# Kernel tuning notes

Hardware: AMD Instinct MI355X
Metric: run time of the kernel (lower is better)

## Reference

```python
import jax, jax.numpy as jnp
import numpy as np

N_NODES = 100000
N_EDGES = 1600000
D = 128
K = 3
LAMBDA_MAX = 2.0  # PyG ChebConv default for normalization='sym'


def _cheb_conv(x, row, col, w, diag, lins, bias):
    # x: [N, D]; w: [E] scaled-Laplacian off-diag weights; diag: scalar diag weight
    # lins: [K, D, D]; bias: [D]
    n = x.shape[0]

    def prop(v):
        # out[col] += w * v[row]  (sparse L_hat @ v), plus diagonal term
        return jax.ops.segment_sum(w[:, None] * v[row], col, num_segments=n) + diag * v

    Tx0 = x
    out = Tx0 @ lins[0]
    Tx1 = prop(Tx0)
    out = out + Tx1 @ lins[1]
    for k in range(2, lins.shape[0]):
        Tx2 = 2.0 * prop(Tx1) - Tx0
        out = out + Tx2 @ lins[k]
        Tx0, Tx1 = Tx1, Tx2
    return out + bias


def setup_inputs() -> dict:
    key = jax.random.key(0)
    ks = jax.random.split(key, 10)
    glorot = float(np.sqrt(6.0 / (D + D)))
    X = jax.random.normal(ks[0], (N_NODES, D), dtype=jnp.float32)
    edge_index = jax.random.randint(ks[1], (2, N_EDGES), 0, N_NODES, dtype=jnp.int64)
    edge_weight = jax.random.uniform(ks[2], (N_EDGES,), dtype=jnp.float32)
    H = jax.random.normal(ks[3], (N_NODES, D), dtype=jnp.float32)
    C = jax.random.normal(ks[4], (N_NODES, D), dtype=jnp.float32)
    # gate order: i, f, c, o
    W = jax.random.uniform(ks[5], (4, D, D), dtype=jnp.float32, minval=-glorot, maxval=glorot)
    b = jnp.zeros((4, D), dtype=jnp.float32)
    conv_W = jax.random.uniform(ks[6], (4, K, D, D), dtype=jnp.float32, minval=-glorot, maxval=glorot)
    conv_b = jnp.zeros((4, D), dtype=jnp.float32)
    return {"X": X, "edge_index": edge_index, "edge_weight": edge_weight,
            "H": H, "C": C, "W": W, "b": b, "conv_W": conv_W, "conv_b": conv_b}


def reference(X, edge_index, edge_weight, H, C, W, b, conv_W, conv_b):
    n = X.shape[0]
    row, col = edge_index[0], edge_index[1]
    # sym-normalized Laplacian, scaled: L_hat = 2L/lmax - I
    deg = jax.ops.segment_sum(edge_weight, row, num_segments=n)
    dinv = jnp.where(deg > 0, deg ** -0.5, 0.0)
    w = -(dinv[row] * edge_weight * dinv[col]) * (2.0 / LAMBDA_MAX)
    diag = 2.0 / LAMBDA_MAX - 1.0  # scalar (0.0 when lmax == 2)

    def gate(g):
        return X @ W[g] + _cheb_conv(H, row, col, w, diag, conv_W[g], conv_b[g]) + b[g]

    I = jax.nn.sigmoid(gate(0))
    F = jax.nn.sigmoid(gate(1))
    T = jnp.tanh(gate(2))
    C_new = F * C + I * T
    O = jax.nn.sigmoid(gate(3))
    H_new = O * jnp.tanh(C_new)
    return H_new
```

## Files before the change

kernel.cpp:

```cpp
#include <hip/hip_runtime.h>

#define N_NODES 100000
#define N_EDGES 1600000
#define CAP 64

typedef unsigned short ushort_t;
typedef __attribute__((ext_vector_type(8))) short bf16x8;
typedef __attribute__((ext_vector_type(4))) float f32x4;
typedef __attribute__((ext_vector_type(4))) int int4e;
typedef __attribute__((ext_vector_type(4))) unsigned short ushort4e;

__device__ __forceinline__ unsigned short f2bf(float f) {
  unsigned int u = __float_as_uint(f);
  u = (u + 0x7FFFu + ((u >> 16) & 1u)) >> 16;
  return (unsigned short)u;
}

__global__ __launch_bounds__(256) void k_misc(
    const int* __restrict__ ei, const float* __restrict__ ew,
    const float* __restrict__ X, const float* __restrict__ H,
    float* __restrict__ deg, int* __restrict__ cnt, int2* __restrict__ bE,
    ushort_t* __restrict__ U,
    const float* __restrict__ W, const float* __restrict__ b,
    const float* __restrict__ cW, const float* __restrict__ cb,
    ushort_t* __restrict__ Bt, float* __restrict__ bias) {
  int bid = blockIdx.x;
  int role = bid & 7, q = bid >> 3;
  if (role < 2) {
    int e = (q * 2 + role) * 256 + threadIdx.x;
    if (e < N_EDGES) atomicAdd(&deg[ei[e]], ew[e]);
  } else if (role < 4) {
    int e = (q * 2 + (role - 2)) * 256 + threadIdx.x;
    if (e < N_EDGES) {
      int r = ei[e], c = ei[N_EDGES + e];
      float w = ew[e];
      int pos = atomicAdd(&cnt[c], 1);
      if (pos < CAP) bE[c * CAP + pos] = make_int2(r, __float_as_int(w));
    }
  } else {
    int s = q * 4 + (role - 4);
    if (s < 12500) {
      int i = s * 256 + threadIdx.x;
      int n = i >> 5, qq = i & 31;
      float4 x = *(const float4*)(X + (size_t)n * 128 + qq * 4);
      float4 h = *(const float4*)(H + (size_t)n * 128 + qq * 4);
      ushort4 a, bb;
      a.x = f2bf(x.x); a.y = f2bf(x.y); a.z = f2bf(x.z); a.w = f2bf(x.w);
      bb.x = f2bf(h.x); bb.y = f2bf(h.y); bb.z = f2bf(h.z); bb.w = f2bf(h.w);
      *(ushort4*)(U + (size_t)n * 512 + qq * 4) = a;
      *(ushort4*)(U + (size_t)n * 512 + 128 + qq * 4) = bb;
    } else if (s < 13524) {
      int idx = (s - 12500) * 256 + threadIdx.x;
      int j = idx >> 9, k = idx & 511;
      int dd = j >> 2, g = j & 3;
      float v;
      if (k < 128) v = W[(g * 128 + k) * 128 + dd];
      else {
        int kk = k - 128;
        int blk = kk >> 7;
        v = cW[((g * 3 + blk) * 128 + (kk & 127)) * 128 + dd];
      }
      Bt[idx] = f2bf(v);
      if (k == 0) bias[j] = b[g * 128 + dd] + cb[g * 128 + dd];
    }
  }
}

__global__ __launch_bounds__(256) void k_scale(
    const int* __restrict__ cnt, const float* __restrict__ deg,
    int2* __restrict__ bE) {
  int slot = blockIdx.x * 256 + threadIdx.x;
  int node = slot >> 6, i = slot & 63;
  int cn = cnt[node]; if (cn > CAP) cn = CAP;
  if (i < cn) {
    int2 p = bE[slot];
    float d = deg[p.x];
    float w = d > 0.f ? rsqrtf(d) * __int_as_float(p.y) : 0.f;
    bE[slot].y = __float_as_int(w);
  }
}

#define FMA4(A, W, V) \
  A.x = fmaf(W, V.x, A.x); A.y = fmaf(W, V.y, A.y); \
  A.z = fmaf(W, V.z, A.z); A.w = fmaf(W, V.w, A.w);

#define GATH(vv, p) { \
  ushort4 rw = *(const ushort4*)(sb + (size_t)(p) * 512); \
  vv.x = __uint_as_float((unsigned)rw.x << 16); \
  vv.y = __uint_as_float((unsigned)rw.y << 16); \
  vv.z = __uint_as_float((unsigned)rw.z << 16); \
  vv.w = __uint_as_float((unsigned)rw.w << 16); }

template <int PHASE>
__global__ __launch_bounds__(256) void k_gather(
    const int* __restrict__ cnt, const int2* __restrict__ bE,
    const float* __restrict__ deg, const float* __restrict__ H,
    ushort_t* __restrict__ U) {
  int g = threadIdx.x >> 5, lane = threadIdx.x & 31;
  int node = blockIdx.x * 8 + g;
  if (node >= N_NODES) return;
  int cn = cnt[node]; if (cn > CAP) cn = CAP;
  const int2* be = bE + node * CAP;
  const ushort_t* sb = U + (PHASE == 1 ? 128 : 256) + lane * 4;
  float dc = deg[node];
  float sc = dc > 0.f ? -rsqrtf(dc) : 0.f;

  float4 z = {0.f, 0.f, 0.f, 0.f};
  float4 a0 = z, a1 = z, a2 = z, a3 = z, a4 = z, a5 = z, a6 = z, a7 = z;
  int i = 0;
  for (; i + 8 <= cn; i += 8) {
    int4e p0 = __builtin_nontemporal_load((const int4e*)(be + i));
    int4e p1 = __builtin_nontemporal_load((const int4e*)(be + i + 2));
    int4e p2 = __builtin_nontemporal_load((const int4e*)(be + i + 4));
    int4e p3 = __builtin_nontemporal_load((const int4e*)(be + i + 6));
    float4 v0, v1, v2, v3, v4, v5, v6, v7;
    GATH(v0, p0.x); GATH(v1, p0.z); GATH(v2, p1.x); GATH(v3, p1.z);
    GATH(v4, p2.x); GATH(v5, p2.z); GATH(v6, p3.x); GATH(v7, p3.z);
    FMA4(a0, __int_as_float(p0.y), v0); FMA4(a1, __int_as_float(p0.w), v1);
    FMA4(a2, __int_as_float(p1.y), v2); FMA4(a3, __int_as_float(p1.w), v3);
    FMA4(a4, __int_as_float(p2.y), v4); FMA4(a5, __int_as_float(p2.w), v5);
    FMA4(a6, __int_as_float(p3.y), v6); FMA4(a7, __int_as_float(p3.w), v7);
  }
  for (; i + 4 <= cn; i += 4) {
    int4e p0 = __builtin_nontemporal_load((const int4e*)(be + i));
    int4e p1 = __builtin_nontemporal_load((const int4e*)(be + i + 2));
    float4 v0, v1, v2, v3;
    GATH(v0, p0.x); GATH(v1, p0.z); GATH(v2, p1.x); GATH(v3, p1.z);
    FMA4(a0, __int_as_float(p0.y), v0); FMA4(a1, __int_as_float(p0.w), v1);
    FMA4(a2, __int_as_float(p1.y), v2); FMA4(a3, __int_as_float(p1.w), v3);
  }
  for (; i < cn; ++i) {
    int2 p = be[i];
    float4 v;
    GATH(v, p.x);
    FMA4(a0, __int_as_float(p.y), v);
  }
  float4 acc;
  acc.x = sc * (((a0.x + a1.x) + (a2.x + a3.x)) + ((a4.x + a5.x) + (a6.x + a7.x)));
  acc.y = sc * (((a0.y + a1.y) + (a2.y + a3.y)) + ((a4.y + a5.y) + (a6.y + a7.y)));
  acc.z = sc * (((a0.z + a1.z) + (a2.z + a3.z)) + ((a4.z + a5.z) + (a6.z + a7.z)));
  acc.w = sc * (((a0.w + a1.w) + (a2.w + a3.w)) + ((a4.w + a5.w) + (a6.w + a7.w)));

  if (PHASE == 1) {
    ushort4e u = {f2bf(acc.x), f2bf(acc.y), f2bf(acc.z), f2bf(acc.w)};
    __builtin_nontemporal_store(u, (ushort4e*)(U + (size_t)node * 512 + 256 + lane * 4));
  } else {
    float4 h = *(const float4*)(H + (size_t)node * 128 + lane * 4);
    ushort4e u = {f2bf(2.f * acc.x - h.x), f2bf(2.f * acc.y - h.y),
                  f2bf(2.f * acc.z - h.z), f2bf(2.f * acc.w - h.w)};
    __builtin_nontemporal_store(u, (ushort4e*)(U + (size_t)node * 512 + 384 + lane * 4));
  }
}

__global__ __launch_bounds__(256) void k_gemm(
    const ushort_t* __restrict__ U, const ushort_t* __restrict__ Bt,
    const float* __restrict__ bias, const float* __restrict__ C,
    float* __restrict__ out) {
  __shared__ char ldsRaw[65536];
  char* ldsA0 = ldsRaw;
  char* ldsB0 = ldsRaw + 16384;
  char* ldsA1 = ldsRaw + 32768;
  char* ldsB1 = ldsRaw + 49152;
  float* ldsF = (float*)ldsRaw;

  const int tid = threadIdx.x;
  const int lane = tid & 63;
  const int w = tid >> 6;
  const int wr = w >> 1, wc = w & 1;
  const int b = blockIdx.x;
  const int g = (b & 7) * 391 + (b >> 3);
  const int m0 = (g >> 2) * 128;
  const int n0 = (g & 3) * 128;
  const int l15 = lane & 15;
  const int l4 = lane >> 4;

  auto stage_half = [&](int kt, char* la_base, char* lb_base, int h) {
    const int k0 = kt * 64;
#pragma unroll
    for (int is = 2 * h; is < 2 * h + 2; ++is) {
      int s = is * 256 + tid;
      int row = s >> 3;
      int cs = (s & 7) ^ (row & 7);
      const ushort_t* ga = U + (size_t)(m0 + row) * 512 + k0 + cs * 8;
      const ushort_t* gb = Bt + (size_t)(n0 + row) * 512 + k0 + cs * 8;
      char* la = la_base + (is * 256 + (tid & 192)) * 16;
      char* lb = lb_base + (is * 256 + (tid & 192)) * 16;
      __builtin_amdgcn_global_load_lds((const __attribute__((address_space(1))) void*)ga,
                                       (__attribute__((address_space(3))) void*)la, 16, 0, 0);
      __builtin_amdgcn_global_load_lds((const __attribute__((address_space(1))) void*)gb,
                                       (__attribute__((address_space(3))) void*)lb, 16, 0, 0);
    }
  };

  const int fcol = tid & 31;
  const int rbase = tid >> 5;
  float cpre[16];
#pragma unroll
  for (int half = 0; half < 2; ++half)
#pragma unroll
    for (int k = 0; k < 8; ++k) {
      int n = m0 + half * 64 + rbase + k * 8;
      int dg = (n0 >> 2) + fcol;
      cpre[half * 8 + k] = (n < N_NODES)
          ? __builtin_nontemporal_load(C + (size_t)n * 128 + dg) : 0.f;
    }

  int offA[2][4], offB[2][4];
#pragma unroll
  for (int ks = 0; ks < 2; ++ks) {
    int slot = ((ks * 4 + l4) ^ (l15 & 7)) * 16;
#pragma unroll
    for (int i = 0; i < 4; ++i) {
      offA[ks][i] = (wr * 64 + i * 16 + l15) * 128 + slot;
      offB[ks][i] = (wc * 64 + i * 16 + l15) * 128 + slot;
    }
  }

  f32x4 acc[4][4] = {};

  stage_half(0, ldsA0, ldsB0, 0);
  stage_half(0, ldsA0, ldsB0, 1);

  for (int kt = 0; kt < 8; ++kt) {
    char* curA = (kt & 1) ? ldsA1 : ldsA0;
    char* curB = (kt & 1) ? ldsB1 : ldsB0;
    char* nA = (kt & 1) ? ldsA0 : ldsA1;
    char* nB = (kt & 1) ? ldsB0 : ldsB1;
    if (kt < 7) {
      stage_half(kt + 1, nA, nB, 0);
      asm volatile("s_waitcnt vmcnt(4)" ::: "memory");
    } else {
      asm volatile("s_waitcnt vmcnt(0)" ::: "memory");
    }
    __builtin_amdgcn_s_barrier();
    __builtin_amdgcn_sched_barrier(0);

    {
      bf16x8 af[4], bfr[4];
#pragma unroll
      for (int mi = 0; mi < 4; ++mi) af[mi] = *(const bf16x8*)(curA + offA[0][mi]);
#pragma unroll
      for (int ni = 0; ni < 4; ++ni) bfr[ni] = *(const bf16x8*)(curB + offB[0][ni]);
      asm volatile("s_waitcnt lgkmcnt(0)" ::: "memory");
      __builtin_amdgcn_sched_barrier(0);
      __builtin_amdgcn_s_setprio(1);
#pragma unroll
      for (int mi = 0; mi < 4; ++mi)
#pragma unroll
        for (int ni = 0; ni < 4; ++ni)
          acc[mi][ni] = __builtin_amdgcn_mfma_f32_16x16x32_bf16(af[mi], bfr[ni], acc[mi][ni], 0, 0, 0);
      __builtin_amdgcn_s_setprio(0);
    }
    if (kt < 7) stage_half(kt + 1, nA, nB, 1);
    {
      bf16x8 af[4], bfr[4];
#pragma unroll
      for (int mi = 0; mi < 4; ++mi) af[mi] = *(const bf16x8*)(curA + offA[1][mi]);
#pragma unroll
      for (int ni = 0; ni < 4; ++ni) bfr[ni] = *(const bf16x8*)(curB + offB[1][ni]);
      asm volatile("s_waitcnt lgkmcnt(0)" ::: "memory");
      __builtin_amdgcn_sched_barrier(0);
      __builtin_amdgcn_s_setprio(1);
#pragma unroll
      for (int mi = 0; mi < 4; ++mi)
#pragma unroll
        for (int ni = 0; ni < 4; ++ni)
          acc[mi][ni] = __builtin_amdgcn_mfma_f32_16x16x32_bf16(af[mi], bfr[ni], acc[mi][ni], 0, 0, 0);
      __builtin_amdgcn_s_setprio(0);
    }
    __builtin_amdgcn_s_barrier();
  }

#pragma unroll
  for (int half = 0; half < 2; ++half) {
    if (wr == half) {
#pragma unroll
      for (int ni = 0; ni < 4; ++ni) {
        int col = wc * 64 + ni * 16 + l15;
        float bv = bias[n0 + col];
#pragma unroll
        for (int mi = 0; mi < 4; ++mi)
#pragma unroll
          for (int r = 0; r < 4; ++r)
            ldsF[(mi * 16 + l4 * 4 + r) * 132 + col] = acc[mi][ni][r] + bv;
      }
    }
    __syncthreads();
#pragma unroll
    for (int k = 0; k < 8; ++k) {
      int p = tid + k * 256;
      int rl = p >> 5, f = p & 31;
      int n = m0 + half * 64 + rl;
      if (n < N_NODES) {
        float4 pre = *(const float4*)&ldsF[rl * 132 + f * 4];
        int dg = (n0 >> 2) + f;
        float ig = __builtin_amdgcn_rcpf(1.f + __expf(-pre.x));
        float fg = __builtin_amdgcn_rcpf(1.f + __expf(-pre.y));
        float ec = __expf(-2.f * fabsf(pre.z));
        float tg = __builtin_copysignf((1.f - ec) * __builtin_amdgcn_rcpf(1.f + ec), pre.z);
        float og = __builtin_amdgcn_rcpf(1.f + __expf(-pre.w));
        float cOld = cpre[half * 8 + k];
        float cn = fg * cOld + ig * tg;
        float en = __expf(-2.f * fabsf(cn));
        float th = __builtin_copysignf((1.f - en) * __builtin_amdgcn_rcpf(1.f + en), cn);
        __builtin_nontemporal_store(og * th, out + (size_t)n * 128 + dg);
      }
    }
    __syncthreads();
  }
}

extern "C" void kernel_launch(void* const* d_in, const int* in_sizes, int n_in,
                              void* d_out, int out_size, void* d_ws, size_t ws_size,
                              hipStream_t stream) {
  const float* X  = (const float*)d_in[0];
  const int*   ei = (const int*)d_in[1];
  const float* ew = (const float*)d_in[2];
  const float* H  = (const float*)d_in[3];
  const float* C  = (const float*)d_in[4];
  const float* W  = (const float*)d_in[5];
  const float* b  = (const float*)d_in[6];
  const float* cW = (const float*)d_in[7];
  const float* cb = (const float*)d_in[8];
  float* out = (float*)d_out;
  char* ws = (char*)d_ws;

  float*    deg  = (float*)(ws);
  int*      cnt  = (int*)(ws + 0x80000);
  int2*     bE   = (int2*)(ws + 0x100000);
  ushort_t* U    = (ushort_t*)(ws + 0x3500000);
  ushort_t* Bt   = (ushort_t*)(ws + 0x9700000);
  float*    bias = (float*)(ws + 0x9780000);

  hipMemsetAsync(ws, 0, 0x100000, stream);

  k_misc<<<27128, 256, 0, stream>>>(ei, ew, X, H, deg, cnt, bE, U, W, b, cW, cb, Bt, bias);
  k_scale<<<N_NODES * CAP / 256, 256, 0, stream>>>(cnt, deg, bE);
  k_gather<1><<<(N_NODES + 7) / 8, 256, 0, stream>>>(cnt, bE, deg, H, U);
  k_gather<2><<<(N_NODES + 7) / 8, 256, 0, stream>>>(cnt, bE, deg, H, U);
  k_gemm<<<3128, 256, 0, stream>>>(U, Bt, bias, C, out);
}
```

Baseline: 449.8 us.

## Widen gather loads to 16 bytes per lane and split degree atomics into two arrays

The gather kernel now assigns 16 lanes per node, each loading 8 bf16 values (16 bytes) per neighbor row instead of 4, so each block processes twice as many nodes and issues fewer, wider loads. The degree accumulation is split across two partial arrays written by different block roles, and a new small kernel sums them, with the aim of reducing atomic contention. The change adds an extra kernel launch and larger memset, and doubles per-thread accumulator registers, which may lower occupancy.

```diff
diff --git a/kernel.cpp b/kernel.cpp
--- a/kernel.cpp
+++ b/kernel.cpp
@@ -8,7 +8,7 @@
 typedef __attribute__((ext_vector_type(8))) short bf16x8;
 typedef __attribute__((ext_vector_type(4))) float f32x4;
 typedef __attribute__((ext_vector_type(4))) int int4e;
-typedef __attribute__((ext_vector_type(4))) unsigned short ushort4e;
+typedef __attribute__((ext_vector_type(8))) unsigned short ushort8e;
 
 __device__ __forceinline__ unsigned short f2bf(float f) {
   unsigned int u = __float_as_uint(f);
@@ -19,7 +19,8 @@
 __global__ __launch_bounds__(256) void k_misc(
     const int* __restrict__ ei, const float* __restrict__ ew,
     const float* __restrict__ X, const float* __restrict__ H,
-    float* __restrict__ deg, int* __restrict__ cnt, int2* __restrict__ bE,
+    float* __restrict__ degc0, float* __restrict__ degc1,
+    int* __restrict__ cnt, int2* __restrict__ bE,
     ushort_t* __restrict__ U,
     const float* __restrict__ W, const float* __restrict__ b,
     const float* __restrict__ cW, const float* __restrict__ cb,
@@ -28,7 +29,10 @@
   int role = bid & 7, q = bid >> 3;
   if (role < 2) {
     int e = (q * 2 + role) * 256 + threadIdx.x;
-    if (e < N_EDGES) atomicAdd(&deg[ei[e]], ew[e]);
+    if (e < N_EDGES) {
+      float* dg = role ? degc1 : degc0;
+      atomicAdd(&dg[ei[e]], ew[e]);
+    }
   } else if (role < 4) {
     int e = (q * 2 + (role - 2)) * 256 + threadIdx.x;
     if (e < N_EDGES) {
@@ -66,6 +70,13 @@
   }
 }
 
+__global__ __launch_bounds__(256) void k_sumdeg(
+    const float* __restrict__ degc0, const float* __restrict__ degc1,
+    float* __restrict__ deg) {
+  int i = blockIdx.x * 256 + threadIdx.x;
+  deg[i] = degc0[i] + degc1[i];
+}
+
 __global__ __launch_bounds__(256) void k_scale(
     const int* __restrict__ cnt, const float* __restrict__ deg,
     int2* __restrict__ bE) {
@@ -80,75 +91,86 @@
   }
 }
 
-#define FMA4(A, W, V) \
-  A.x = fmaf(W, V.x, A.x); A.y = fmaf(W, V.y, A.y); \
-  A.z = fmaf(W, V.z, A.z); A.w = fmaf(W, V.w, A.w);
-
-#define GATH(vv, p) { \
-  ushort4 rw = *(const ushort4*)(sb + (size_t)(p) * 512); \
-  vv.x = __uint_as_float((unsigned)rw.x << 16); \
-  vv.y = __uint_as_float((unsigned)rw.y << 16); \
-  vv.z = __uint_as_float((unsigned)rw.z << 16); \
-  vv.w = __uint_as_float((unsigned)rw.w << 16); }
+#define FMA8(A, Wt, R) { \
+  A[0] = fmaf(Wt, __uint_as_float((unsigned)R.x << 16), A[0]); \
+  A[1] = fmaf(Wt, __uint_as_float((unsigned)R.x & 0xffff0000u), A[1]); \
+  A[2] = fmaf(Wt, __uint_as_float((unsigned)R.y << 16), A[2]); \
+  A[3] = fmaf(Wt, __uint_as_float((unsigned)R.y & 0xffff0000u), A[3]); \
+  A[4] = fmaf(Wt, __uint_as_float((unsigned)R.z << 16), A[4]); \
+  A[5] = fmaf(Wt, __uint_as_float((unsigned)R.z & 0xffff0000u), A[5]); \
+  A[6] = fmaf(Wt, __uint_as_float((unsigned)R.w << 16), A[6]); \
+  A[7] = fmaf(Wt, __uint_as_float((unsigned)R.w & 0xffff0000u), A[7]); }
 
 template <int PHASE>
 __global__ __launch_bounds__(256) void k_gather(
     const int* __restrict__ cnt, const int2* __restrict__ bE,
     const float* __restrict__ deg, const float* __restrict__ H,
     ushort_t* __restrict__ U) {
-  int g = threadIdx.x >> 5, lane = threadIdx.x & 31;
-  int node = blockIdx.x * 8 + g;
+  int g = threadIdx.x >> 4, lane = threadIdx.x & 15;
+  int node = blockIdx.x * 16 + g;
   if (node >= N_NODES) return;
   int cn = cnt[node]; if (cn > CAP) cn = CAP;
   const int2* be = bE + node * CAP;
-  const ushort_t* sb = U + (PHASE == 1 ? 128 : 256) + lane * 4;
+  const ushort_t* sb = U + (PHASE == 1 ? 128 : 256) + lane * 8;
   float dc = deg[node];
   float sc = dc > 0.f ? -rsqrtf(dc) : 0.f;
 
-  float4 z = {0.f, 0.f, 0.f, 0.f};
-  float4 a0 = z, a1 = z, a2 = z, a3 = z, a4 = z, a5 = z, a6 = z, a7 = z;
+  float a0[8] = {}, a1[8] = {}, a2[8] = {}, a3[8] = {};
+  float a4[8] = {}, a5[8] = {}, a6[8] = {}, a7[8] = {};
   int i = 0;
   for (; i + 8 <= cn; i += 8) {
     int4e p0 = __builtin_nontemporal_load((const int4e*)(be + i));
     int4e p1 = __builtin_nontemporal_load((const int4e*)(be + i + 2));
     int4e p2 = __builtin_nontemporal_load((const int4e*)(be + i + 4));
     int4e p3 = __builtin_nontemporal_load((const int4e*)(be + i + 6));
-    float4 v0, v1, v2, v3, v4, v5, v6, v7;
-    GATH(v0, p0.x); GATH(v1, p0.z); GATH(v2, p1.x); GATH(v3, p1.z);
-    GATH(v4, p2.x); GATH(v5, p2.z); GATH(v6, p3.x); GATH(v7, p3.z);
-    FMA4(a0, __int_as_float(p0.y), v0); FMA4(a1, __int_as_float(p0.w), v1);
-    FMA4(a2, __int_as_float(p1.y), v2); FMA4(a3, __int_as_float(p1.w), v3);
-    FMA4(a4, __int_as_float(p2.y), v4); FMA4(a5, __int_as_float(p2.w), v5);
-    FMA4(a6, __int_as_float(p3.y), v6); FMA4(a7, __int_as_float(p3.w), v7);
+    int4e r0 = *(const int4e*)(sb + (size_t)p0.x * 512);
+    int4e r1 = *(const int4e*)(sb + (size_t)p0.z * 512);
+    int4e r2 = *(const int4e*)(sb + (size_t)p1.x * 512);
+    int4e r3 = *(const int4e*)(sb + (size_t)p1.z * 512);
+    int4e r4 = *(const int4e*)(sb + (size_t)p2.x * 512);
+    int4e r5 = *(const int4e*)(sb + (size_t)p2.z * 512);
+    int4e r6 = *(const int4e*)(sb + (size_t)p3.x * 512);
+    int4e r7 = *(const int4e*)(sb + (size_t)p3.z * 512);
+    FMA8(a0, __int_as_float(p0.y), r0); FMA8(a1, __int_as_float(p0.w), r1);
+    FMA8(a2, __int_as_float(p1.y), r2); FMA8(a3, __int_as_float(p1.w), r3);
+    FMA8(a4, __int_as_float(p2.y), r4); FMA8(a5, __int_as_float(p2.w), r5);
+    FMA8(a6, __int_as_float(p3.y), r6); FMA8(a7, __int_as_float(p3.w), r7);
   }
   for (; i + 4 <= cn; i += 4) {
     int4e p0 = __builtin_nontemporal_load((const int4e*)(be + i));
     int4e p1 = __builtin_nontemporal_load((const int4e*)(be + i + 2));
-    float4 v0, v1, v2, v3;
-    GATH(v0, p0.x); GATH(v1, p0.z); GATH(v2, p1.x); GATH(v3, p1.z);
-    FMA4(a0, __int_as_float(p0.y), v0); FMA4(a1, __int_as_float(p0.w), v1);
-    FMA4(a2, __int_as_float(p1.y), v2); FMA4(a3, __int_as_float(p1.w), v3);
+    int4e r0 = *(const int4e*)(sb + (size_t)p0.x * 512);
+    int4e r1 = *(const int4e*)(sb + (size_t)p0.z * 512);
+    int4e r2 = *(const int4e*)(sb + (size_t)p1.x * 512);
+    int4e r3 = *(const int4e*)(sb + (size_t)p1.z * 512);
+    FMA8(a0, __int_as_float(p0.y), r0); FMA8(a1, __int_as_float(p0.w), r1);
+    FMA8(a2, __int_as_float(p1.y), r2); FMA8(a3, __int_as_float(p1.w), r3);
   }
   for (; i < cn; ++i) {
     int2 p = be[i];
-    float4 v;
-    GATH(v, p.x);
-    FMA4(a0, __int_as_float(p.y), v);
-  }
-  float4 acc;
-  acc.x = sc * (((a0.x + a1.x) + (a2.x + a3.x)) + ((a4.x + a5.x) + (a6.x + a7.x)));
-  acc.y = sc * (((a0.y + a1.y) + (a2.y + a3.y)) + ((a4.y + a5.y) + (a6.y + a7.y)));
-  acc.z = sc * (((a0.z + a1.z) + (a2.z + a3.z)) + ((a4.z + a5.z) + (a6.z + a7.z)));
-  acc.w = sc * (((a0.w + a1.w) + (a2.w + a3.w)) + ((a4.w + a5.w) + (a6.w + a7.w)));
+    int4e r0 = *(const int4e*)(sb + (size_t)p.x * 512);
+    FMA8(a0, __int_as_float(p.y), r0);
+  }
+  float o[8];
+#pragma unroll
+  for (int j = 0; j < 8; ++j)
+    o[j] = sc * (((a0[j] + a1[j]) + (a2[j] + a3[j])) +
+                 ((a4[j] + a5[j]) + (a6[j] + a7[j])));
 
   if (PHASE == 1) {
-    ushort4e u = {f2bf(acc.x), f2bf(acc.y), f2bf(acc.z), f2bf(acc.w)};
-    __builtin_nontemporal_store(u, (ushort4e*)(U + (size_t)node * 512 + 256 + lane * 4));
+    ushort8e u;
+#pragma unroll
+    for (int j = 0; j < 8; ++j) u[j] = f2bf(o[j]);
+    __builtin_nontemporal_store(u, (ushort8e*)(U + (size_t)node * 512 + 256 + lane * 8));
   } else {
-    float4 h = *(const float4*)(H + (size_t)node * 128 + lane * 4);
-    ushort4e u = {f2bf(2.f * acc.x - h.x), f2bf(2.f * acc.y - h.y),
-                  f2bf(2.f * acc.z - h.z), f2bf(2.f * acc.w - h.w)};
-    __builtin_nontemporal_store(u, (ushort4e*)(U + (size_t)node * 512 + 384 + lane * 4));
+    float4 hlo = *(const float4*)(H + (size_t)node * 128 + lane * 8);
+    float4 hhi = *(const float4*)(H + (size_t)node * 128 + lane * 8 + 4);
+    ushort8e u;
+    u[0] = f2bf(2.f * o[0] - hlo.x); u[1] = f2bf(2.f * o[1] - hlo.y);
+    u[2] = f2bf(2.f * o[2] - hlo.z); u[3] = f2bf(2.f * o[3] - hlo.w);
+    u[4] = f2bf(2.f * o[4] - hhi.x); u[5] = f2bf(2.f * o[5] - hhi.y);
+    u[6] = f2bf(2.f * o[6] - hhi.z); u[7] = f2bf(2.f * o[7] - hhi.w);
+    __builtin_nontemporal_store(u, (ushort8e*)(U + (size_t)node * 512 + 384 + lane * 8));
   }
 }
 
@@ -325,18 +347,22 @@
   float* out = (float*)d_out;
   char* ws = (char*)d_ws;
 
-  float*    deg  = (float*)(ws);
-  int*      cnt  = (int*)(ws + 0x80000);
-  int2*     bE   = (int2*)(ws + 0x100000);
-  ushort_t* U    = (ushort_t*)(ws + 0x3500000);
-  ushort_t* Bt   = (ushort_t*)(ws + 0x9700000);
-  float*    bias = (float*)(ws + 0x9780000);
-
-  hipMemsetAsync(ws, 0, 0x100000, stream);
-
-  k_misc<<<27128, 256, 0, stream>>>(ei, ew, X, H, deg, cnt, bE, U, W, b, cW, cb, Bt, bias);
+  float*    degc0 = (float*)(ws);
+  float*    degc1 = (float*)(ws + 0x80000);
+  float*    deg   = (float*)(ws + 0x100000);
+  int*      cnt   = (int*)(ws + 0x180000);
+  int2*     bE    = (int2*)(ws + 0x200000);
+  ushort_t* U     = (ushort_t*)(ws + 0x3600000);
+  ushort_t* Bt    = (ushort_t*)(ws + 0x9800000);
+  float*    bias  = (float*)(ws + 0x9880000);
+
+  hipMemsetAsync(ws, 0, 0x200000, stream);
+
+  k_misc<<<27128, 256, 0, stream>>>(ei, ew, X, H, degc0, degc1, cnt, bE, U,
+                                    W, b, cW, cb, Bt, bias);
+  k_sumdeg<<<392, 256, 0, stream>>>(degc0, degc1, deg);
   k_scale<<<N_NODES * CAP / 256, 256, 0, stream>>>(cnt, deg, bE);
-  k_gather<1><<<(N_NODES + 7) / 8, 256, 0, stream>>>(cnt, bE, deg, H, U);
-  k_gather<2><<<(N_NODES + 7) / 8, 256, 0, stream>>>(cnt, bE, deg, H, U);
+  k_gather<1><<<(N_NODES + 15) / 16, 256, 0, stream>>>(cnt, bE, deg, H, U);
+  k_gather<2><<<(N_NODES + 15) / 16, 256, 0, stream>>>(cnt, bE, deg, H, U);
   k_gemm<<<3128, 256, 0, stream>>>(U, Bt, bias, C, out);
 }
```

After: 424.3 us. 1.06x faster.
